# Performance work log

Hardware: AMD Instinct MI355X
Metric: run time of the kernel (lower is better)

## Reference

```python
import jax, jax.numpy as jnp
import numpy as np

N_HEADS = 16
N_EMB = 1024
HEAD_SIZE = 64
BLOCK_SIZE = 2048


def setup_inputs() -> dict:
    key = jax.random.key(0)
    k1, k2, k3, k4, k5 = jax.random.split(key, 5)
    B, T, E, H, D = 4, BLOCK_SIZE, N_EMB, N_HEADS, HEAD_SIZE
    s = 1.0 / np.sqrt(E)
    x = jax.random.normal(k1, (B, T, E), dtype=jnp.float32)
    # Stacked per-head projection weights (Linear with bias=False): [H, E, D]
    Wq = jax.random.normal(k2, (H, E, D), dtype=jnp.float32) * s
    Wk = jax.random.normal(k3, (H, E, D), dtype=jnp.float32) * s
    Wv = jax.random.normal(k4, (H, E, D), dtype=jnp.float32) * s
    Wo = jax.random.normal(k5, (H * D, E), dtype=jnp.float32) * (1.0 / np.sqrt(H * D))
    return {"x": x, "Wq": Wq, "Wk": Wk, "Wv": Wv, "Wo": Wo}


def reference(x, Wq, Wk, Wv, Wo):
    # x: [B,T,E]; Wq/Wk/Wv: [H,E,D]; Wo: [H*D,E]
    B, T, E = x.shape
    H, _, D = Wq.shape
    q = jnp.einsum('bte,hed->bhtd', x, Wq)
    k = jnp.einsum('bte,hed->bhtd', x, Wk)
    v = jnp.einsum('bte,hed->bhtd', x, Wv)
    scores = jnp.einsum('bhtd,bhsd->bhts', q, k) * (D ** -0.5)  # [B,H,T,T]
    causal = jnp.tril(jnp.ones((T, T), dtype=bool))
    scores = jnp.where(causal, scores, -jnp.inf)
    wei = jax.nn.softmax(scores, axis=-1)  # dropout is identity in eval mode
    out = jnp.einsum('bhts,bhsd->bhtd', wei, v)  # [B,H,T,D]
    out = out.transpose(0, 2, 1, 3).reshape(B, T, H * D)  # concat heads
    return out @ Wo  # [B,T,E]
```

## Files before the change

### kernel.cpp

```cpp
#include <hip/hip_runtime.h>

#define B_  4
#define T_  2048
#define E_  1024
#define H_  16
#define D_  64
#define HD_ 1024
#define BT_ 8192

typedef __bf16 bf16x8 __attribute__((ext_vector_type(8)));
typedef float  f32x4  __attribute__((ext_vector_type(4)));

static __device__ __forceinline__ unsigned short f2bf(float f) {
  __bf16 h = (__bf16)f;
  return __builtin_bit_cast(unsigned short, h);
}
static __device__ __forceinline__ bf16x8 ldb8(const unsigned short* p) {
  return *(const bf16x8*)p;
}

#define GLD_LDS16(gp, lp)                                                      \
  __builtin_amdgcn_global_load_lds(                                            \
      (const __attribute__((address_space(1))) void*)(gp),                     \
      (__attribute__((address_space(3))) void*)(lp), 16, 0, 0)

__global__ __launch_bounds__(256) void prep_k(const float* __restrict__ x,
                                              const float* __restrict__ Wq,
                                              const float* __restrict__ Wk,
                                              const float* __restrict__ Wv,
                                              const float* __restrict__ Wo,
                                              unsigned short* __restrict__ xb,
                                              unsigned short* __restrict__ wT,
                                              unsigned short* __restrict__ woT) {
  const int bid = blockIdx.x, tid = threadIdx.x;
  if (bid < 2048) {
    #pragma unroll
    for (int p = 0; p < 4; ++p) {
      int i = bid * 1024 + p * 256 + tid;
      float4 v = ((const float4*)x)[i];
      ushort4 o;
      o.x = f2bf(v.x); o.y = f2bf(v.y); o.z = f2bf(v.z); o.w = f2bf(v.w);
      ((ushort4*)xb)[i] = o;
    }
    return;
  }
  __shared__ float tl[64 * 65];
  if (bid < 2816) {
    const int tix = bid - 2048;
    const int w = tix >> 8;
    const int h = (tix >> 4) & 15;
    const int e0 = (tix & 15) * 64;
    const float* src = (w == 0) ? Wq : (w == 1) ? Wk : Wv;
    #pragma unroll
    for (int rr = 0; rr < 4; ++rr) {
      const int e = e0 + rr * 16 + (tid >> 4);
      const int d4 = (tid & 15) * 4;
      float4 v = *(const float4*)&src[(size_t)(h * 1024 + e) * 64 + d4];
      tl[(e - e0) * 65 + d4 + 0] = v.x;
      tl[(e - e0) * 65 + d4 + 1] = v.y;
      tl[(e - e0) * 65 + d4 + 2] = v.z;
      tl[(e - e0) * 65 + d4 + 3] = v.w;
    }
    __syncthreads();
    #pragma unroll
    for (int cc = 0; cc < 4; ++cc) {
      const int d = cc * 16 + (tid >> 4);
      const int e4 = (tid & 15) * 4;
      ushort4 o;
      o.x = f2bf(tl[(e4 + 0) * 65 + d]);
      o.y = f2bf(tl[(e4 + 1) * 65 + d]);
      o.z = f2bf(tl[(e4 + 2) * 65 + d]);
      o.w = f2bf(tl[(e4 + 3) * 65 + d]);
      *(ushort4*)&wT[(size_t)((w * 16 + h) * 64 + d) * 1024 + e0 + e4] = o;
    }
    return;
  }
  {
    const int tix = bid - 2816;
    const int hd0 = (tix >> 4) * 64;
    const int e0 = (tix & 15) * 64;
    #pragma unroll
    for (int rr = 0; rr < 4; ++rr) {
      const int hd = hd0 + rr * 16 + (tid >> 4);
      const int e4 = (tid & 15) * 4;
      float4 v = *(const float4*)&Wo[(size_t)hd * 1024 + e0 + e4];
      tl[(hd - hd0) * 65 + e4 + 0] = v.x;
      tl[(hd - hd0) * 65 + e4 + 1] = v.y;
      tl[(hd - hd0) * 65 + e4 + 2] = v.z;
      tl[(hd - hd0) * 65 + e4 + 3] = v.w;
    }
    __syncthreads();
    #pragma unroll
    for (int cc = 0; cc < 4; ++cc) {
      const int e = e0 + cc * 16 + (tid >> 4);
      const int hd4 = (tid & 15) * 4;
      ushort4 o;
      o.x = f2bf(tl[(hd4 + 0) * 65 + (e - e0)]);
      o.y = f2bf(tl[(hd4 + 1) * 65 + (e - e0)]);
      o.z = f2bf(tl[(hd4 + 2) * 65 + (e - e0)]);
      o.w = f2bf(tl[(hd4 + 3) * 65 + (e - e0)]);
      *(ushort4*)&woT[(size_t)e * 1024 + hd0 + hd4] = o;
    }
  }
}

static __device__ __forceinline__ void gemm_core(const unsigned short* __restrict__ A,
                                                 const unsigned short* __restrict__ BT,
                                                 const int K, const int m0, const int n0,
                                                 unsigned short* lA, unsigned short* lB,
                                                 f32x4 acc[4][2]) {
  const int tid  = threadIdx.x;
  const int wave = tid >> 6;
  const int lane = tid & 63;
  const int wm = wave & 1, wn = wave >> 1;
  const int l16 = lane & 15, quad = lane >> 4;
  const int nit = K >> 5;

  const int sr = tid >> 2;
  const int sc = ((tid & 3) ^ ((sr >> 1) & 3)) * 8;
  const int slot = (quad ^ ((l16 >> 1) & 3)) << 3;

#define STG(kt) do {                                                            \
    const size_t kb = (size_t)(kt) * 32 + sc;                                   \
    unsigned short* dA = lA + ((kt) & 1) * 4096 + wave * 512;                   \
    unsigned short* dB = lB + ((kt) & 1) * 2048 + wave * 512;                   \
    GLD_LDS16(A  + (size_t)(m0 +      sr) * K + kb, dA);                        \
    GLD_LDS16(A  + (size_t)(m0 + 64 + sr) * K + kb, dA + 2048);                 \
    GLD_LDS16(BT + (size_t)(n0 +      sr) * K + kb, dB);                        \
  } while (0)

  #pragma unroll
  for (int i = 0; i < 4; ++i)
    #pragma unroll
    for (int j = 0; j < 2; ++j) acc[i][j] = (f32x4){0.f, 0.f, 0.f, 0.f};

  STG(0);
  for (int kt = 0; kt < nit; ++kt) {
    __syncthreads();
    if (kt + 1 < nit) STG(kt + 1);
    const unsigned short* cA = lA + (kt & 1) * 4096;
    const unsigned short* cB = lB + (kt & 1) * 2048;
    bf16x8 aF[4], bF[2];
    #pragma unroll
    for (int mi = 0; mi < 4; ++mi)
      aF[mi] = ldb8(cA + (wm * 64 + mi * 16 + l16) * 32 + slot);
    #pragma unroll
    for (int nj = 0; nj < 2; ++nj)
      bF[nj] = ldb8(cB + (wn * 32 + nj * 16 + l16) * 32 + slot);
    __builtin_amdgcn_s_setprio(1);
    #pragma unroll
    for (int mi = 0; mi < 4; ++mi)
      #pragma unroll
      for (int nj = 0; nj < 2; ++nj)
        acc[mi][nj] = __builtin_amdgcn_mfma_f32_16x16x32_bf16(aF[mi], bF[nj],
                                                              acc[mi][nj], 0, 0, 0);
    __builtin_amdgcn_s_setprio(0);
  }
#undef STG
}

__global__ __launch_bounds__(256) void qkv_gemm_k(const unsigned short* __restrict__ xb,
                                                  const unsigned short* __restrict__ wT,
                                                  unsigned short* __restrict__ q,
                                                  unsigned short* __restrict__ k,
                                                  unsigned short* __restrict__ vT) {
  __shared__ unsigned short lA[2 * 128 * 32];
  __shared__ unsigned short lB[2 * 64 * 32];
  f32x4 acc[4][2];
  const int m0 = blockIdx.x * 128, n0 = blockIdx.y * 64;
  gemm_core(xb, wT, E_, m0, n0, lA, lB, acc);

  const int wave = threadIdx.x >> 6, lane = threadIdx.x & 63;
  const int wm = wave & 1, wn = wave >> 1;
  const int l16 = lane & 15, quad = lane >> 4;
  const int type = n0 >> 10;
  const float C = 0.18033688011112042f;
  #pragma unroll
  for (int i = 0; i < 4; ++i) {
    #pragma unroll
    for (int j = 0; j < 2; ++j) {
      const int n = n0 + wn * 32 + j * 16 + l16;
      const int h = (n >> 6) & 15, d = n & 63;
      #pragma unroll
      for (int r = 0; r < 4; ++r) {
        const int m = m0 + wm * 64 + i * 16 + quad * 4 + r;
        const int b = m >> 11, t = m & (T_ - 1);
        if (type == 0)
          q[((size_t)(b * H_ + h) * T_ + t) * D_ + d] = f2bf(acc[i][j][r] * C);
        else if (type == 1)
          k[((size_t)(b * H_ + h) * T_ + t) * D_ + d] = f2bf(acc[i][j][r]);
        else
          vT[((size_t)(b * H_ + h) * D_ + d) * T_ + t] = f2bf(acc[i][j][r]);
      }
    }
  }
}

__global__ __launch_bounds__(256) void proj_k(const unsigned short* __restrict__ ao,
                                              const unsigned short* __restrict__ woT,
                                              float* __restrict__ out) {
  __shared__ unsigned short lA[2 * 128 * 32];
  __shared__ unsigned short lB[2 * 64 * 32];
  f32x4 acc[4][2];
  const int m0 = blockIdx.x * 128, n0 = blockIdx.y * 64;
  gemm_core(ao, woT, HD_, m0, n0, lA, lB, acc);

  const int wave = threadIdx.x >> 6, lane = threadIdx.x & 63;
  const int wm = wave & 1, wn = wave >> 1;
  const int l16 = lane & 15, quad = lane >> 4;
  #pragma unroll
  for (int i = 0; i < 4; ++i)
    #pragma unroll
    for (int j = 0; j < 2; ++j)
      #pragma unroll
      for (int r = 0; r < 4; ++r)
        out[(size_t)(m0 + wm * 64 + i * 16 + quad * 4 + r) * E_ +
            n0 + wn * 32 + j * 16 + l16] = acc[i][j][r];
}

__global__ __launch_bounds__(256) void attn_k(const unsigned short* __restrict__ q,
                                              const unsigned short* __restrict__ k,
                                              const unsigned short* __restrict__ vT,
                                              unsigned short* __restrict__ ao) {
  __shared__ unsigned short lK[2][64 * 64];
  __shared__ unsigned short lV[2][64 * 64];
  __shared__ unsigned short lP[4][32][72];
  const int tid  = threadIdx.x;
  const int lane = tid & 63;
  const int wave = tid >> 6;
  const int l16  = lane & 15;
  const int quad = lane >> 4;
  const int id    = (int)blockIdx.x;
  const int bhid  = id & 63;
  const int qpair = id >> 6;
  const int h = bhid & 15, b = bhid >> 4;
  const size_t bh = (size_t)(b * H_ + h);
  const unsigned short* qp = q  + bh * (T_ * D_);
  const unsigned short* kp = k  + bh * (T_ * D_);
  const unsigned short* vp = vT + bh * (D_ * T_);

  const int srow = tid >> 3;
  const int kseg = (tid & 7) ^ (srow & 7);
  const int sw = (l16 & 7);

  #pragma unroll
  for (int pr = 0; pr < 2; ++pr) {
    const int qblk = (pr == 0) ? qpair : 15 - qpair;
    const int q0 = qblk * 128 + wave * 32;

    bf16x8 aq[2][2];
    #pragma unroll
    for (int rb = 0; rb < 2; ++rb)
      #pragma unroll
      for (int hh = 0; hh < 2; ++hh)
        aq[rb][hh] = ldb8(qp + (q0 + rb * 16 + l16) * D_ + hh * 32 + quad * 8);

    float lr[2][4];
    f32x4 o[2][4];
    #pragma unroll
    for (int rb = 0; rb < 2; ++rb) {
      #pragma unroll
      for (int r = 0; r < 4; ++r) lr[rb][r] = 0.f;
      #pragma unroll
      for (int nb = 0; nb < 4; ++nb) o[rb][nb] = (f32x4){0.f, 0.f, 0.f, 0.f};
    }

    const int nch = 2 * (qblk + 1);

    {
      unsigned short* Kb = lK[0];
      unsigned short* Vb = lV[0];
      GLD_LDS16(kp + srow * D_ + kseg * 8, Kb + wave * 512);
      GLD_LDS16(kp + (32 + srow) * D_ + kseg * 8, Kb + 2048 + wave * 512);
      GLD_LDS16(vp + (size_t)srow * T_ + kseg * 8, Vb + wave * 512);
      GLD_LDS16(vp + (size_t)(32 + srow) * T_ + kseg * 8, Vb + 2048 + wave * 512);
    }

    for (int c = 0; c < nch; ++c) {
      __syncthreads();
      if (c + 1 < nch) {
        const int s1 = (c + 1) * 64;
        unsigned short* Kb = lK[(c + 1) & 1];
        unsigned short* Vb = lV[(c + 1) & 1];
        GLD_LDS16(kp + (s1 + srow) * D_ + kseg * 8, Kb + wave * 512);
        GLD_LDS16(kp + (s1 + 32 + srow) * D_ + kseg * 8, Kb + 2048 + wave * 512);
        GLD_LDS16(vp + (size_t)srow * T_ + s1 + kseg * 8, Vb + wave * 512);
        GLD_LDS16(vp + (size_t)(32 + srow) * T_ + s1 + kseg * 8, Vb + 2048 + wave * 512);
      }
      const int s0 = c * 64;
      const unsigned short* Kb = lK[c & 1];
      const unsigned short* Vb = lV[c & 1];
      f32x4 sc[2][4];
      #pragma unroll
      for (int rb = 0; rb < 2; ++rb)
        #pragma unroll
        for (int j = 0; j < 4; ++j) sc[rb][j] = (f32x4){0.f, 0.f, 0.f, 0.f};
      #pragma unroll
      for (int j = 0; j < 4; ++j) {
        const int sr = j * 16 + l16;
        bf16x8 bk0 = ldb8(Kb + sr * 64 + ((quad ^ sw) << 3));
        bf16x8 bk1 = ldb8(Kb + sr * 64 + (((4 + quad) ^ sw) << 3));
        #pragma unroll
        for (int rb = 0; rb < 2; ++rb) {
          sc[rb][j] = __builtin_amdgcn_mfma_f32_16x16x32_bf16(aq[rb][0], bk0, sc[rb][j], 0, 0, 0);
          sc[rb][j] = __builtin_amdgcn_mfma_f32_16x16x32_bf16(aq[rb][1], bk1, sc[rb][j], 0, 0, 0);
        }
      }
      const bool domask = (c == nch - 1) || (c == nch - 2);
      #pragma unroll
      for (int rb = 0; rb < 2; ++rb) {
        #pragma unroll
        for (int j = 0; j < 4; ++j) {
          #pragma unroll
          for (int r = 0; r < 4; ++r) {
            float p = __builtin_amdgcn_exp2f(sc[rb][j][r]);
            if (domask) {
              const int qg = q0 + rb * 16 + quad * 4 + r;
              if (s0 + j * 16 + l16 > qg) p = 0.f;
            }
            lr[rb][r] += p;
            lP[wave][rb * 16 + quad * 4 + r][j * 16 + l16] = f2bf(p);
          }
        }
      }
      __builtin_amdgcn_wave_barrier();
      bf16x8 aP[2][2];
      #pragma unroll
      for (int rb = 0; rb < 2; ++rb)
        #pragma unroll
        for (int hh = 0; hh < 2; ++hh)
          aP[rb][hh] = ldb8(&lP[wave][rb * 16 + l16][hh * 32 + quad * 8]);
      __builtin_amdgcn_wave_barrier();
      #pragma unroll
      for (int nb = 0; nb < 4; ++nb) {
        const int d = nb * 16 + l16;
        bf16x8 bV0 = ldb8(Vb + d * 64 + ((quad ^ sw) << 3));
        bf16x8 bV1 = ldb8(Vb + d * 64 + (((4 + quad) ^ sw) << 3));
        #pragma unroll
        for (int rb = 0; rb < 2; ++rb) {
          o[rb][nb] = __builtin_amdgcn_mfma_f32_16x16x32_bf16(aP[rb][0], bV0, o[rb][nb], 0, 0, 0);
          o[rb][nb] = __builtin_amdgcn_mfma_f32_16x16x32_bf16(aP[rb][1], bV1, o[rb][nb], 0, 0, 0);
        }
      }
    }

    #pragma unroll
    for (int off = 1; off < 16; off <<= 1)
      #pragma unroll
      for (int rb = 0; rb < 2; ++rb)
        #pragma unroll
        for (int r = 0; r < 4; ++r)
          lr[rb][r] += __shfl_xor(lr[rb][r], off, 64);
    #pragma unroll
    for (int rb = 0; rb < 2; ++rb) {
      #pragma unroll
      for (int r = 0; r < 4; ++r) {
        const float inv = 1.0f / lr[rb][r];
        const int t = q0 + rb * 16 + quad * 4 + r;
        #pragma unroll
        for (int nb = 0; nb < 4; ++nb)
          ao[((size_t)(b * T_ + t) * H_ + h) * D_ + nb * 16 + l16] = f2bf(o[rb][nb][r] * inv);
      }
    }
  }
}


extern "C" void kernel_launch(void* const* d_in, const int* in_sizes, int n_in,
                              void* d_out, int out_size, void* d_ws, size_t ws_size,
                              hipStream_t stream) {
  const float* x  = (const float*)d_in[0];
  const float* Wq = (const float*)d_in[1];
  const float* Wk = (const float*)d_in[2];
  const float* Wv = (const float*)d_in[3];
  const float* Wo = (const float*)d_in[4];
  float* out = (float*)d_out;

  char* ws = (char*)d_ws;
  unsigned short* xb   = (unsigned short*)(ws + 0);
  unsigned short* wT   = (unsigned short*)(ws + 16777216);
  unsigned short* woT  = (unsigned short*)(ws + 23068672);
  unsigned short* qb   = (unsigned short*)(ws + 25165824);
  unsigned short* kb   = (unsigned short*)(ws + 41943040);
  unsigned short* vTb  = (unsigned short*)(ws + 58720256);
  unsigned short* aob  = (unsigned short*)(ws + 75497472);

  prep_k<<<dim3(3072), dim3(256), 0, stream>>>(x, Wq, Wk, Wv, Wo, xb, wT, woT);
  qkv_gemm_k<<<dim3(BT_ / 128, 3072 / 64), dim3(256), 0, stream>>>(xb, wT, qb, kb, vTb);
  attn_k<<<dim3(512), dim3(256), 0, stream>>>(qb, kb, vTb, aob);
  proj_k<<<dim3(BT_ / 128, E_ / 64), dim3(256), 0, stream>>>(aob, woT, out);
}
```

Baseline: 284.3 us.

## Triple-buffer GEMM and attention staging, widen GEMM tiles to 128x128

The shared GEMM core now uses three LDS stages with a prefetch distance of two and explicit vmcnt waits. Its output tile grows from 128x64 to 128x128, so each wave computes a 64x64 sub-tile and A-fragment reuse doubles. The attention kernel's K/V chunk staging likewise moves from double to triple buffering, with the per-chunk barrier moved to the end of the chunk. The aim is to hide global-to-LDS load latency and cut global traffic per FLOP. The cost is more LDS and registers per block, which can lower occupancy, and the GEMM grids now launch half as many blocks.

```diff
diff --git a/kernel.cpp b/kernel.cpp
--- a/kernel.cpp
+++ b/kernel.cpp
@@ -108,7 +108,7 @@
                                                  const unsigned short* __restrict__ BT,
                                                  const int K, const int m0, const int n0,
                                                  unsigned short* lA, unsigned short* lB,
-                                                 f32x4 acc[4][2]) {
+                                                 f32x4 acc[4][4]) {
   const int tid  = threadIdx.x;
   const int wave = tid >> 6;
   const int lane = tid & 63;
@@ -120,41 +120,55 @@
   const int sc = ((tid & 3) ^ ((sr >> 1) & 3)) * 8;
   const int slot = (quad ^ ((l16 >> 1) & 3)) << 3;
 
-#define STG(kt) do {                                                            \
+#define STG(kt, bi) do {                                                        \
     const size_t kb = (size_t)(kt) * 32 + sc;                                   \
-    unsigned short* dA = lA + ((kt) & 1) * 4096 + wave * 512;                   \
-    unsigned short* dB = lB + ((kt) & 1) * 2048 + wave * 512;                   \
+    unsigned short* dA = lA + (bi) * 4096 + wave * 512;                         \
+    unsigned short* dB = lB + (bi) * 4096 + wave * 512;                         \
     GLD_LDS16(A  + (size_t)(m0 +      sr) * K + kb, dA);                        \
     GLD_LDS16(A  + (size_t)(m0 + 64 + sr) * K + kb, dA + 2048);                 \
     GLD_LDS16(BT + (size_t)(n0 +      sr) * K + kb, dB);                        \
+    GLD_LDS16(BT + (size_t)(n0 + 64 + sr) * K + kb, dB + 2048);                 \
   } while (0)
 
   #pragma unroll
   for (int i = 0; i < 4; ++i)
     #pragma unroll
-    for (int j = 0; j < 2; ++j) acc[i][j] = (f32x4){0.f, 0.f, 0.f, 0.f};
-
-  STG(0);
-  for (int kt = 0; kt < nit; ++kt) {
-    __syncthreads();
-    if (kt + 1 < nit) STG(kt + 1);
-    const unsigned short* cA = lA + (kt & 1) * 4096;
-    const unsigned short* cB = lB + (kt & 1) * 2048;
-    bf16x8 aF[4], bF[2];
+    for (int j = 0; j < 4; ++j) acc[i][j] = (f32x4){0.f, 0.f, 0.f, 0.f};
+
+  STG(0, 0);
+  STG(1, 1);
+  asm volatile("s_waitcnt vmcnt(4)" ::: "memory");
+  __builtin_amdgcn_s_barrier();
+
+  int cb = 0, sb = 2;
+  for (int it = 0; it < nit; ++it) {
+    if (it + 2 < nit) STG(it + 2, sb);
+    const unsigned short* cA = lA + cb * 4096;
+    const unsigned short* cB = lB + cb * 4096;
+    bf16x8 aF[4], bF[4];
     #pragma unroll
     for (int mi = 0; mi < 4; ++mi)
       aF[mi] = ldb8(cA + (wm * 64 + mi * 16 + l16) * 32 + slot);
     #pragma unroll
-    for (int nj = 0; nj < 2; ++nj)
-      bF[nj] = ldb8(cB + (wn * 32 + nj * 16 + l16) * 32 + slot);
+    for (int nj = 0; nj < 4; ++nj)
+      bF[nj] = ldb8(cB + (wn * 64 + nj * 16 + l16) * 32 + slot);
     __builtin_amdgcn_s_setprio(1);
     #pragma unroll
     for (int mi = 0; mi < 4; ++mi)
       #pragma unroll
-      for (int nj = 0; nj < 2; ++nj)
+      for (int nj = 0; nj < 4; ++nj)
         acc[mi][nj] = __builtin_amdgcn_mfma_f32_16x16x32_bf16(aF[mi], bF[nj],
                                                               acc[mi][nj], 0, 0, 0);
     __builtin_amdgcn_s_setprio(0);
+    if (it + 1 < nit) {
+      if (it + 2 < nit)
+        asm volatile("s_waitcnt vmcnt(4)" ::: "memory");
+      else
+        asm volatile("s_waitcnt vmcnt(0)" ::: "memory");
+      __builtin_amdgcn_s_barrier();
+    }
+    cb = (cb == 2) ? 0 : cb + 1;
+    sb = (sb == 2) ? 0 : sb + 1;
   }
 #undef STG
 }
@@ -164,10 +178,9 @@
                                                   unsigned short* __restrict__ q,
                                                   unsigned short* __restrict__ k,
                                                   unsigned short* __restrict__ vT) {
-  __shared__ unsigned short lA[2 * 128 * 32];
-  __shared__ unsigned short lB[2 * 64 * 32];
-  f32x4 acc[4][2];
-  const int m0 = blockIdx.x * 128, n0 = blockIdx.y * 64;
+  __shared__ unsigned short lA[3 * 128 * 32], lB[3 * 128 * 32];
+  f32x4 acc[4][4];
+  const int m0 = blockIdx.x * 128, n0 = blockIdx.y * 128;
   gemm_core(xb, wT, E_, m0, n0, lA, lB, acc);
 
   const int wave = threadIdx.x >> 6, lane = threadIdx.x & 63;
@@ -178,8 +191,8 @@
   #pragma unroll
   for (int i = 0; i < 4; ++i) {
     #pragma unroll
-    for (int j = 0; j < 2; ++j) {
-      const int n = n0 + wn * 32 + j * 16 + l16;
+    for (int j = 0; j < 4; ++j) {
+      const int n = n0 + wn * 64 + j * 16 + l16;
       const int h = (n >> 6) & 15, d = n & 63;
       #pragma unroll
       for (int r = 0; r < 4; ++r) {
@@ -199,10 +212,9 @@
 __global__ __launch_bounds__(256) void proj_k(const unsigned short* __restrict__ ao,
                                               const unsigned short* __restrict__ woT,
                                               float* __restrict__ out) {
-  __shared__ unsigned short lA[2 * 128 * 32];
-  __shared__ unsigned short lB[2 * 64 * 32];
-  f32x4 acc[4][2];
-  const int m0 = blockIdx.x * 128, n0 = blockIdx.y * 64;
+  __shared__ unsigned short lA[3 * 128 * 32], lB[3 * 128 * 32];
+  f32x4 acc[4][4];
+  const int m0 = blockIdx.x * 128, n0 = blockIdx.y * 128;
   gemm_core(ao, woT, HD_, m0, n0, lA, lB, acc);
 
   const int wave = threadIdx.x >> 6, lane = threadIdx.x & 63;
@@ -211,19 +223,19 @@
   #pragma unroll
   for (int i = 0; i < 4; ++i)
     #pragma unroll
-    for (int j = 0; j < 2; ++j)
+    for (int j = 0; j < 4; ++j)
       #pragma unroll
       for (int r = 0; r < 4; ++r)
         out[(size_t)(m0 + wm * 64 + i * 16 + quad * 4 + r) * E_ +
-            n0 + wn * 32 + j * 16 + l16] = acc[i][j][r];
+            n0 + wn * 64 + j * 16 + l16] = acc[i][j][r];
 }
 
 __global__ __launch_bounds__(256) void attn_k(const unsigned short* __restrict__ q,
                                               const unsigned short* __restrict__ k,
                                               const unsigned short* __restrict__ vT,
                                               unsigned short* __restrict__ ao) {
-  __shared__ unsigned short lK[2][64 * 64];
-  __shared__ unsigned short lV[2][64 * 64];
+  __shared__ unsigned short lK[3][64 * 64];
+  __shared__ unsigned short lV[3][64 * 64];
   __shared__ unsigned short lP[4][32][72];
   const int tid  = threadIdx.x;
   const int lane = tid & 63;
@@ -243,11 +255,23 @@
   const int kseg = (tid & 7) ^ (srow & 7);
   const int sw = (l16 & 7);
 
+#define STAGE_CH(cc) do {                                                       \
+    const int s1 = (cc) * 64;                                                   \
+    unsigned short* Kb = lK[(cc) % 3];                                          \
+    unsigned short* Vb = lV[(cc) % 3];                                          \
+    GLD_LDS16(kp + (s1 + srow) * D_ + kseg * 8, Kb + wave * 512);               \
+    GLD_LDS16(kp + (s1 + 32 + srow) * D_ + kseg * 8, Kb + 2048 + wave * 512);   \
+    GLD_LDS16(vp + (size_t)srow * T_ + s1 + kseg * 8, Vb + wave * 512);         \
+    GLD_LDS16(vp + (size_t)(32 + srow) * T_ + s1 + kseg * 8, Vb + 2048 + wave * 512); \
+  } while (0)
+
   #pragma unroll
   for (int pr = 0; pr < 2; ++pr) {
     const int qblk = (pr == 0) ? qpair : 15 - qpair;
     const int q0 = qblk * 128 + wave * 32;
 
+    __syncthreads();
+
     bf16x8 aq[2][2];
     #pragma unroll
     for (int rb = 0; rb < 2; ++rb)
@@ -267,29 +291,17 @@
 
     const int nch = 2 * (qblk + 1);
 
-    {
-      unsigned short* Kb = lK[0];
-      unsigned short* Vb = lV[0];
-      GLD_LDS16(kp + srow * D_ + kseg * 8, Kb + wave * 512);
-      GLD_LDS16(kp + (32 + srow) * D_ + kseg * 8, Kb + 2048 + wave * 512);
-      GLD_LDS16(vp + (size_t)srow * T_ + kseg * 8, Vb + wave * 512);
-      GLD_LDS16(vp + (size_t)(32 + srow) * T_ + kseg * 8, Vb + 2048 + wave * 512);
-    }
+    STAGE_CH(0);
+    STAGE_CH(1);
+    asm volatile("s_waitcnt vmcnt(4)" ::: "memory");
+    __builtin_amdgcn_s_barrier();
+    asm volatile("" ::: "memory");
 
     for (int c = 0; c < nch; ++c) {
-      __syncthreads();
-      if (c + 1 < nch) {
-        const int s1 = (c + 1) * 64;
-        unsigned short* Kb = lK[(c + 1) & 1];
-        unsigned short* Vb = lV[(c + 1) & 1];
-        GLD_LDS16(kp + (s1 + srow) * D_ + kseg * 8, Kb + wave * 512);
-        GLD_LDS16(kp + (s1 + 32 + srow) * D_ + kseg * 8, Kb + 2048 + wave * 512);
-        GLD_LDS16(vp + (size_t)srow * T_ + s1 + kseg * 8, Vb + wave * 512);
-        GLD_LDS16(vp + (size_t)(32 + srow) * T_ + s1 + kseg * 8, Vb + 2048 + wave * 512);
-      }
+      if (c + 2 < nch) STAGE_CH(c + 2);
       const int s0 = c * 64;
-      const unsigned short* Kb = lK[c & 1];
-      const unsigned short* Vb = lV[c & 1];
+      const unsigned short* Kb = lK[c % 3];
+      const unsigned short* Vb = lV[c % 3];
       f32x4 sc[2][4];
       #pragma unroll
       for (int rb = 0; rb < 2; ++rb)
@@ -342,6 +354,12 @@
           o[rb][nb] = __builtin_amdgcn_mfma_f32_16x16x32_bf16(aP[rb][1], bV1, o[rb][nb], 0, 0, 0);
         }
       }
+      if (c + 2 < nch)
+        asm volatile("s_waitcnt vmcnt(4)" ::: "memory");
+      else if (c + 1 < nch)
+        asm volatile("s_waitcnt vmcnt(0)" ::: "memory");
+      __builtin_amdgcn_s_barrier();
+      asm volatile("" ::: "memory");
     }
 
     #pragma unroll
@@ -363,6 +381,7 @@
       }
     }
   }
+#undef STAGE_CH
 }
 
 
@@ -386,7 +405,7 @@
   unsigned short* aob  = (unsigned short*)(ws + 75497472);
 
   prep_k<<<dim3(3072), dim3(256), 0, stream>>>(x, Wq, Wk, Wv, Wo, xb, wT, woT);
-  qkv_gemm_k<<<dim3(BT_ / 128, 3072 / 64), dim3(256), 0, stream>>>(xb, wT, qb, kb, vTb);
+  qkv_gemm_k<<<dim3(BT_ / 128, 3072 / 128), dim3(256), 0, stream>>>(xb, wT, qb, kb, vTb);
   attn_k<<<dim3(512), dim3(256), 0, stream>>>(qb, kb, vTb, aob);
-  proj_k<<<dim3(BT_ / 128, E_ / 64), dim3(256), 0, stream>>>(aob, woT, out);
-}
+  proj_k<<<dim3(BT_ / 128, E_ / 128), dim3(256), 0, stream>>>(aob, woT, out);
+}
```

Measured after the change: 257.1 us. 1.11x faster.
